# Optimization experiments

Measured on AMD Instinct MI355X. Metric: run time of the kernel, lower is better.

## Reference

```python
import jax, jax.numpy as jnp
import numpy as np

B, S, T = 512, 1024, 48
START, STOP, PAD = 45, 46, 47
NEG = -10000.0


def setup_inputs() -> dict:
    key = jax.random.key(0)
    k1, k2, k3, k4 = jax.random.split(key, 4)
    feats = jax.random.normal(k1, (B, S, T), dtype=jnp.float32)
    # contiguous-prefix masks (lengths in [1, S]) as the torch code assumes
    lengths = jax.random.randint(k2, (B,), 1, S + 1)
    masks = (jnp.arange(S)[None, :] < lengths[:, None]).astype(jnp.float32)
    tags = jax.random.randint(k3, (B, S), 0, T - 3)  # real tags only
    # transitions[i, j] = score of transitioning from tag j to tag i
    trans = jax.random.normal(k4, (T, T), dtype=jnp.float32)
    trans = trans.at[START, :].set(NEG)
    trans = trans.at[:, STOP].set(NEG)
    trans = trans.at[:, PAD].set(NEG)
    trans = trans.at[PAD, :].set(NEG)
    trans = trans.at[PAD, STOP].set(0.0)
    trans = trans.at[PAD, PAD].set(0.0)
    return {"feats": feats, "masks": masks, "tags": tags, "transitions": trans}


def _forward_algo(feats, masks, transitions):
    # feats [B,S,T], masks [B,S] -> partition log Z per sequence [B]
    score0 = jnp.full(feats.shape[::2], NEG, dtype=feats.dtype).at[:, START].set(0.0)

    def step(score, xs):
        emit, m = xs  # emit [B,T], m [B,1]
        # new[b,i] = LSE_j(score[b,j] + trans[i,j]) + emit[b,i]
        new = jax.nn.logsumexp(score[:, None, :] + transitions[None, :, :], axis=2) + emit
        return new * m + score * (1.0 - m), None

    xs = (jnp.swapaxes(feats, 0, 1), masks.T[:, :, None])
    score, _ = jax.lax.scan(step, score0, xs)
    return jax.nn.logsumexp(score + transitions[STOP][None, :], axis=1)


def _score_sentence(feats, masks, tags, transitions):
    # gold path score, vectorized over batch and time
    Bb = masks.shape[0]
    tags_ext = jnp.concatenate(
        [jnp.full((Bb, 1), START, dtype=tags.dtype), tags], axis=1)  # [B,S+1]
    emission = jnp.take_along_axis(feats, tags[:, :, None], axis=2)[:, :, 0]  # [B,S]
    trans_sc = transitions[tags_ext[:, 1:], tags_ext[:, :-1]]  # [B,S]
    score = jnp.sum((emission + trans_sc) * masks, axis=1)
    last_idx = masks.sum(1).astype(jnp.int32)  # length -> index into tags_ext
    last_tags = jnp.take_along_axis(tags_ext, last_idx[:, None], axis=1)[:, 0]
    return score + transitions[STOP, last_tags]


def reference(feats, masks, tags, transitions):
    # standard CRF negative log-likelihood per sequence: logZ - gold score
    return _forward_algo(feats, masks, transitions) - _score_sentence(
        feats, masks, tags, transitions)
```

## Files before the change

kernel.cpp:

```cpp
#include <hip/hip_runtime.h>
#include <cstdint>

constexpr int Sd = 1024;
constexpr int Td = 48;
constexpr int NTAG = 45;
constexpr int START_ = 45;
constexpr int STOP_ = 46;

typedef float v2f __attribute__((ext_vector_type(2)));

__device__ __forceinline__ int rfl_i(int x) { return __builtin_amdgcn_readfirstlane(x); }

#define ROTF(x, c) __int_as_float(__builtin_amdgcn_mov_dpp(__float_as_int(x), 0x120|(c), 0xF, 0xF, false))

#define STEP1(PF) do {                                                         \
    int _vi = __float_as_int(v);                                               \
    int _b1 = __builtin_amdgcn_ds_bpermute(a16, _vi);                          \
    int _b2 = __builtin_amdgcn_ds_bpermute(a32, _vi);                          \
    float _e = __expf(PF);                                                     \
    float g0v[16], g1v[16], g2v[16];                                           \
    g0v[0] = v;                                                                \
    g0v[1] = ROTF(g0v[0], 1);                                                  \
    g0v[2] = ROTF(g0v[0], 2);                                                  \
    g0v[3] = ROTF(g0v[1], 2);                                                  \
    _Pragma("unroll")                                                          \
    for (int i_ = 0; i_ < 4; ++i_) g0v[4+i_] = ROTF(g0v[i_], 4);               \
    _Pragma("unroll")                                                          \
    for (int i_ = 0; i_ < 8; ++i_) g0v[8+i_] = ROTF(g0v[i_], 8);               \
    g1v[0] = __int_as_float(_b1);                                              \
    g1v[1] = ROTF(g1v[0], 1);                                                  \
    g1v[2] = ROTF(g1v[0], 2);                                                  \
    g1v[3] = ROTF(g1v[1], 2);                                                  \
    _Pragma("unroll")                                                          \
    for (int i_ = 0; i_ < 4; ++i_) g1v[4+i_] = ROTF(g1v[i_], 4);               \
    _Pragma("unroll")                                                          \
    for (int i_ = 0; i_ < 8; ++i_) g1v[8+i_] = ROTF(g1v[i_], 8);               \
    g2v[0] = __int_as_float(_b2);                                              \
    g2v[1] = ROTF(g2v[0], 1);                                                  \
    g2v[2] = ROTF(g2v[0], 2);                                                  \
    g2v[3] = ROTF(g2v[1], 2);                                                  \
    _Pragma("unroll")                                                          \
    for (int i_ = 0; i_ < 4; ++i_) g2v[4+i_] = ROTF(g2v[i_], 4);               \
    _Pragma("unroll")                                                          \
    for (int i_ = 0; i_ < 8; ++i_) g2v[8+i_] = ROTF(g2v[i_], 8);               \
    v2f _ac0={0.f,0.f}, _ac1={0.f,0.f}, _ac2={0.f,0.f};                        \
    _Pragma("unroll")                                                          \
    for (int j_ = 0; j_ < 8; ++j_) {                                           \
        v2f _g0 = { g0v[2*j_], g0v[2*j_+1] };                                  \
        v2f _g1 = { g1v[2*j_], g1v[2*j_+1] };                                  \
        v2f _g2 = { g2v[2*j_], g2v[2*j_+1] };                                  \
        _ac0 = __builtin_elementwise_fma(epk[0][j_], _g0, _ac0);               \
        _ac1 = __builtin_elementwise_fma(epk[1][j_], _g1, _ac1);               \
        _ac2 = __builtin_elementwise_fma(epk[2][j_], _g2, _ac2);               \
    }                                                                          \
    v2f _s = _ac0 + (_ac1 + _ac2);                                             \
    float tot_ = _s.x + _s.y;                                                  \
    L += kx;                                                                   \
    uf = tot_ * sc;                                                            \
    v  = tot_ * (_e * sc);                                                     \
    { int _kb = rfl_i(__float_as_int(v));                                      \
      kx = ((_kb >> 23) & 0xFF) - 127;                                         \
      sc = __int_as_float((127 - kx) << 23); }                                 \
} while (0)

#define ADVP() do {                                                            \
    bool ok_ = isb ? (tn > 0) : (tn < tmax);                                   \
    pcur += ok_ ? sAdv : 0;                                                    \
    tn   += ok_ ? sInc : 0;                                                    \
} while (0)

__launch_bounds__(64, 1)
__global__ void crf_chains(const float* __restrict__ feats,
                           const float* __restrict__ masks,
                           const int* __restrict__ tags,
                           const float* __restrict__ trans,
                           float* __restrict__ wsv,
                           float* __restrict__ wsu,
                           int* __restrict__ wsLF, int* __restrict__ wsLB,
                           float* __restrict__ wsg,
                           int Bn)
{
    __shared__ float tl[Td * Td];
    const int lane = threadIdx.x;
    const bool isb = ((int)blockIdx.x >= Bn);
    const int b = isb ? ((int)blockIdx.x - Bn) : (int)blockIdx.x;

    for (int i = lane; i < Td * Td; i += 64) tl[i] = trans[i];
    __syncthreads();

    const size_t bS = (size_t)b * Sd;

    float c = 0.f;
    for (int t = lane; t < Sd; t += 64) c += masks[bS + t];
#pragma unroll
    for (int off = 32; off; off >>= 1) c += __shfl_xor(c, off);
    int len = (int)(c + 0.5f);
    if (len < 1) len = 1;
    len = rfl_i(len);

    if (!isb) {
        float g = 0.f;
        for (int t = lane; t < len; t += 64) {
            const int tag  = tags[bS + t];
            const int prev = (t == 0) ? START_ : tags[bS + t - 1];
            g += feats[(bS + t) * Td + tag] + tl[tag * Td + prev];
        }
#pragma unroll
        for (int off = 32; off; off >>= 1) g += __shfl_xor(g, off);
        g += tl[STOP_ * Td + tags[bS + len - 1]];
        if (lane == 0) wsg[b] = g;
    }

    const int p = lane & 15;
    const int qd = __builtin_amdgcn_mov_dpp(p, 0x121, 0xF, 0xF, false);
    const int d = (qd == ((p + 1) & 15)) ? 1 : -1;
    const int r0 = (lane >> 4) & 3;

    const int a16 = (((lane + 16) % Td) << 2);
    const int a32 = (((lane + 32) % Td) << 2);

    v2f epk[3][8];
#pragma unroll
    for (int h = 0; h < 3; ++h) {
        const int blk = 16 * ((r0 + h) % 3);
#pragma unroll
        for (int j = 0; j < 8; ++j) {
            const int c0 = blk + ((p + d * (2 * j))     & 15);
            const int c1 = blk + ((p + d * (2 * j + 1)) & 15);
            float e0 = 0.f, e1 = 0.f;
            if (!isb) {
                if (lane < NTAG) {
                    e0 = __expf(tl[lane * Td + c0]);
                    e1 = __expf(tl[lane * Td + c1]);
                }
            } else {
                if (lane < Td) {
                    e0 = __expf(tl[c0 * Td + lane]);
                    e1 = __expf(tl[c1 * Td + lane]);
                }
            }
            v2f ee = { e0, e1 };
            epk[h][j] = ee;
        }
    }

    const int lidx = (lane < Td) ? lane : 0;
    const float* frow = feats + bS * Td;
    const int Fh = (len + 1) >> 1;
    const int act = rfl_i(isb ? (len - Fh) : (Fh - 1));
    const int it0 = isb ? (len - 1) : 0;

    float einit;
    if (!isb) einit = (lane < NTAG) ? __expf(tl[lane * Td + START_]) : 0.f;
    else      einit = (lane < Td)   ? __expf(tl[STOP_ * Td + lane])  : 0.f;

    float v  = __expf(frow[(size_t)it0 * Td + lidx]) * einit;
    float uf = einit;
    int L = 0, kx; float sc;
    { int kb = rfl_i(__float_as_int(v)); kx = ((kb >> 23) & 0xFF) - 127;
      sc = __int_as_float((127 - kx) << 23); }

    auto eidx0 = [&](int s) -> int {
        if (!isb) { int t = 1 + s; return t < Sd ? t : (Sd - 1); }
        int t = len - 2 - s; return t > 0 ? t : 0;
    };
    float pf0 = frow[(size_t)eidx0(0) * Td + lidx];
    float pf1 = frow[(size_t)eidx0(1) * Td + lidx];
    float pf2 = frow[(size_t)eidx0(2) * Td + lidx];
    float pf3 = frow[(size_t)eidx0(3) * Td + lidx];
    float pf4 = frow[(size_t)eidx0(4) * Td + lidx];
    float pf5 = frow[(size_t)eidx0(5) * Td + lidx];
    float pf6 = frow[(size_t)eidx0(6) * Td + lidx];
    float pf7 = frow[(size_t)eidx0(7) * Td + lidx];
    int tn = eidx0(8);
    const float* pcur = frow + (size_t)tn * Td;
    const int sAdv = isb ? -Td : Td;
    const int sInc = isb ? -1 : 1;
    const int tmax = Sd - 1;

    int s = 0;
    while (s + 8 <= act) {
        STEP1(pf0); pf0 = pcur[lidx]; ADVP();
        STEP1(pf1); pf1 = pcur[lidx]; ADVP();
        STEP1(pf2); pf2 = pcur[lidx]; ADVP();
        STEP1(pf3); pf3 = pcur[lidx]; ADVP();
        STEP1(pf4); pf4 = pcur[lidx]; ADVP();
        STEP1(pf5); pf5 = pcur[lidx]; ADVP();
        STEP1(pf6); pf6 = pcur[lidx]; ADVP();
        STEP1(pf7); pf7 = pcur[lidx]; ADVP();
        s += 8;
    }
    if (s < act) { STEP1(pf0); ++s; }
    if (s < act) { STEP1(pf1); ++s; }
    if (s < act) { STEP1(pf2); ++s; }
    if (s < act) { STEP1(pf3); ++s; }
    if (s < act) { STEP1(pf4); ++s; }
    if (s < act) { STEP1(pf5); ++s; }
    if (s < act) { STEP1(pf6); ++s; }

    if (!isb) {
        if (lane < Td) wsv[lane * Bn + b] = v;
        if (lane == 0) wsLF[b] = L;
    } else {
        if (lane < Td) wsu[lane * Bn + b] = uf;
        if (lane == 0) wsLB[b] = L;
    }
}

__launch_bounds__(64)
__global__ void crf_combine(const float* __restrict__ wsv,
                            const float* __restrict__ wsu,
                            const int* __restrict__ wsLF,
                            const int* __restrict__ wsLB,
                            const float* __restrict__ wsg,
                            float* __restrict__ out, int Bn)
{
    const int b = blockIdx.x * 64 + threadIdx.x;
    if (b >= Bn) return;
    float dot = 0.f;
#pragma unroll
    for (int j = 0; j < Td; ++j)
        dot += wsv[j * Bn + b] * wsu[j * Bn + b];
    const float ln2 = 0.6931471805599453f;
    out[b] = (float)(wsLF[b] + wsLB[b]) * ln2 + __logf(dot) - wsg[b];
}

extern "C" void kernel_launch(void* const* d_in, const int* in_sizes, int n_in,
                              void* d_out, int out_size, void* d_ws, size_t ws_size,
                              hipStream_t stream) {
    const float* feats = (const float*)d_in[0];
    const float* masks = (const float*)d_in[1];
    const int*   tags  = (const int*)d_in[2];
    const float* trans = (const float*)d_in[3];
    float* outp = (float*)d_out;

    const int Bn = in_sizes[1] / Sd;

    float* wsv  = (float*)d_ws;
    float* wsu  = wsv + (size_t)Td * Bn;
    int*   wsLF = (int*)(wsu + (size_t)Td * Bn);
    int*   wsLB = wsLF + Bn;
    float* wsg  = (float*)(wsLB + Bn);

    crf_chains<<<dim3(2 * Bn), dim3(64), 0, stream>>>(feats, masks, tags, trans,
                                                      wsv, wsu, wsLF, wsLB, wsg, Bn);
    crf_combine<<<dim3((Bn + 63) / 64), dim3(64), 0, stream>>>(wsv, wsu, wsLF, wsLB, wsg, outp, Bn);
}
```

Before: 131.5 us.

## Fold DPP row rotations into FMA operands and hoist emission exp off the chain

Replaces the explicit DPP rotation tree and packed-FMA accumulation with inline-asm v_fmac_f32 instructions that apply row_ror directly to the source operand. Each slot is now 16 DPP-modified FMAs split across two accumulators, so the separate mov_dpp instructions are gone. The exp of the emission scores is computed when the prefetch is issued rather than inside the dependent step. This shortens the serial recurrence latency per time step, at the cost of losing packed v_pk_fma throughput and relying on inline asm that the compiler cannot schedule around.

```diff
diff --git a/kernel.cpp b/kernel.cpp
--- a/kernel.cpp
+++ b/kernel.cpp
@@ -7,57 +7,39 @@
 constexpr int START_ = 45;
 constexpr int STOP_ = 46;
 
-typedef float v2f __attribute__((ext_vector_type(2)));
-
 __device__ __forceinline__ int rfl_i(int x) { return __builtin_amdgcn_readfirstlane(x); }
 
-#define ROTF(x, c) __int_as_float(__builtin_amdgcn_mov_dpp(__float_as_int(x), 0x120|(c), 0xF, 0xF, false))
+#define FMD(acc, s, ee, N) \
+    asm("v_fmac_f32 %0, %1, %2 row_ror:" #N " row_mask:0xf bank_mask:0xf" \
+        : "+v"(acc) : "v"(s), "v"(ee))
+#define MULD(acc, s, ee, N) \
+    asm("v_mul_f32 %0, %1, %2 row_ror:" #N " row_mask:0xf bank_mask:0xf" \
+        : "=v"(acc) : "v"(s), "v"(ee))
+
+#define SLOT16(s, E, aA, aB) do {                                              \
+    aA = (s) * E[0];                                                           \
+    FMD(aA, s, E[1], 1);  FMD(aA, s, E[2], 2);  FMD(aA, s, E[3], 3);           \
+    FMD(aA, s, E[4], 4);  FMD(aA, s, E[5], 5);  FMD(aA, s, E[6], 6);           \
+    FMD(aA, s, E[7], 7);                                                       \
+    MULD(aB, s, E[8], 8);                                                      \
+    FMD(aB, s, E[9], 9);  FMD(aB, s, E[10], 10); FMD(aB, s, E[11], 11);        \
+    FMD(aB, s, E[12], 12); FMD(aB, s, E[13], 13); FMD(aB, s, E[14], 14);       \
+    FMD(aB, s, E[15], 15);                                                     \
+} while (0)
 
 #define STEP1(PF) do {                                                         \
     int _vi = __float_as_int(v);                                               \
     int _b1 = __builtin_amdgcn_ds_bpermute(a16, _vi);                          \
     int _b2 = __builtin_amdgcn_ds_bpermute(a32, _vi);                          \
-    float _e = __expf(PF);                                                     \
-    float g0v[16], g1v[16], g2v[16];                                           \
-    g0v[0] = v;                                                                \
-    g0v[1] = ROTF(g0v[0], 1);                                                  \
-    g0v[2] = ROTF(g0v[0], 2);                                                  \
-    g0v[3] = ROTF(g0v[1], 2);                                                  \
-    _Pragma("unroll")                                                          \
-    for (int i_ = 0; i_ < 4; ++i_) g0v[4+i_] = ROTF(g0v[i_], 4);               \
-    _Pragma("unroll")                                                          \
-    for (int i_ = 0; i_ < 8; ++i_) g0v[8+i_] = ROTF(g0v[i_], 8);               \
-    g1v[0] = __int_as_float(_b1);                                              \
-    g1v[1] = ROTF(g1v[0], 1);                                                  \
-    g1v[2] = ROTF(g1v[0], 2);                                                  \
-    g1v[3] = ROTF(g1v[1], 2);                                                  \
-    _Pragma("unroll")                                                          \
-    for (int i_ = 0; i_ < 4; ++i_) g1v[4+i_] = ROTF(g1v[i_], 4);               \
-    _Pragma("unroll")                                                          \
-    for (int i_ = 0; i_ < 8; ++i_) g1v[8+i_] = ROTF(g1v[i_], 8);               \
-    g2v[0] = __int_as_float(_b2);                                              \
-    g2v[1] = ROTF(g2v[0], 1);                                                  \
-    g2v[2] = ROTF(g2v[0], 2);                                                  \
-    g2v[3] = ROTF(g2v[1], 2);                                                  \
-    _Pragma("unroll")                                                          \
-    for (int i_ = 0; i_ < 4; ++i_) g2v[4+i_] = ROTF(g2v[i_], 4);               \
-    _Pragma("unroll")                                                          \
-    for (int i_ = 0; i_ < 8; ++i_) g2v[8+i_] = ROTF(g2v[i_], 8);               \
-    v2f _ac0={0.f,0.f}, _ac1={0.f,0.f}, _ac2={0.f,0.f};                        \
-    _Pragma("unroll")                                                          \
-    for (int j_ = 0; j_ < 8; ++j_) {                                           \
-        v2f _g0 = { g0v[2*j_], g0v[2*j_+1] };                                  \
-        v2f _g1 = { g1v[2*j_], g1v[2*j_+1] };                                  \
-        v2f _g2 = { g2v[2*j_], g2v[2*j_+1] };                                  \
-        _ac0 = __builtin_elementwise_fma(epk[0][j_], _g0, _ac0);               \
-        _ac1 = __builtin_elementwise_fma(epk[1][j_], _g1, _ac1);               \
-        _ac2 = __builtin_elementwise_fma(epk[2][j_], _g2, _ac2);               \
-    }                                                                          \
-    v2f _s = _ac0 + (_ac1 + _ac2);                                             \
-    float tot_ = _s.x + _s.y;                                                  \
+    float _s1 = __int_as_float(_b1), _s2 = __int_as_float(_b2);                \
+    float a0A, a0B, a1A, a1B, a2A, a2B;                                        \
+    SLOT16(v,   eA0, a0A, a0B);                                                \
+    SLOT16(_s1, eA1, a1A, a1B);                                                \
+    SLOT16(_s2, eA2, a2A, a2B);                                                \
+    float tot_ = ((a0A + a0B) + (a1A + a1B)) + (a2A + a2B);                    \
     L += kx;                                                                   \
     uf = tot_ * sc;                                                            \
-    v  = tot_ * (_e * sc);                                                     \
+    v  = tot_ * ((PF) * sc);                                                   \
     { int _kb = rfl_i(__float_as_int(v));                                      \
       kx = ((_kb >> 23) & 0xFF) - 127;                                         \
       sc = __int_as_float((127 - kx) << 23); }                                 \
@@ -119,28 +101,21 @@
     const int a16 = (((lane + 16) % Td) << 2);
     const int a32 = (((lane + 32) % Td) << 2);
 
-    v2f epk[3][8];
+    float eA0[16], eA1[16], eA2[16];
 #pragma unroll
     for (int h = 0; h < 3; ++h) {
+        float* dst = (h == 0) ? eA0 : (h == 1) ? eA1 : eA2;
         const int blk = 16 * ((r0 + h) % 3);
 #pragma unroll
-        for (int j = 0; j < 8; ++j) {
-            const int c0 = blk + ((p + d * (2 * j))     & 15);
-            const int c1 = blk + ((p + d * (2 * j + 1)) & 15);
-            float e0 = 0.f, e1 = 0.f;
+        for (int i = 0; i < 16; ++i) {
+            const int cc = blk + ((p + d * i) & 15);
+            float e0 = 0.f;
             if (!isb) {
-                if (lane < NTAG) {
-                    e0 = __expf(tl[lane * Td + c0]);
-                    e1 = __expf(tl[lane * Td + c1]);
-                }
+                if (lane < NTAG) e0 = __expf(tl[lane * Td + cc]);
             } else {
-                if (lane < Td) {
-                    e0 = __expf(tl[c0 * Td + lane]);
-                    e1 = __expf(tl[c1 * Td + lane]);
-                }
+                if (lane < Td)   e0 = __expf(tl[cc * Td + lane]);
             }
-            v2f ee = { e0, e1 };
-            epk[h][j] = ee;
+            dst[i] = e0;
         }
     }
 
@@ -164,14 +139,14 @@
         if (!isb) { int t = 1 + s; return t < Sd ? t : (Sd - 1); }
         int t = len - 2 - s; return t > 0 ? t : 0;
     };
-    float pf0 = frow[(size_t)eidx0(0) * Td + lidx];
-    float pf1 = frow[(size_t)eidx0(1) * Td + lidx];
-    float pf2 = frow[(size_t)eidx0(2) * Td + lidx];
-    float pf3 = frow[(size_t)eidx0(3) * Td + lidx];
-    float pf4 = frow[(size_t)eidx0(4) * Td + lidx];
-    float pf5 = frow[(size_t)eidx0(5) * Td + lidx];
-    float pf6 = frow[(size_t)eidx0(6) * Td + lidx];
-    float pf7 = frow[(size_t)eidx0(7) * Td + lidx];
+    float pf0 = __expf(frow[(size_t)eidx0(0) * Td + lidx]);
+    float pf1 = __expf(frow[(size_t)eidx0(1) * Td + lidx]);
+    float pf2 = __expf(frow[(size_t)eidx0(2) * Td + lidx]);
+    float pf3 = __expf(frow[(size_t)eidx0(3) * Td + lidx]);
+    float pf4 = __expf(frow[(size_t)eidx0(4) * Td + lidx]);
+    float pf5 = __expf(frow[(size_t)eidx0(5) * Td + lidx]);
+    float pf6 = __expf(frow[(size_t)eidx0(6) * Td + lidx]);
+    float pf7 = __expf(frow[(size_t)eidx0(7) * Td + lidx]);
     int tn = eidx0(8);
     const float* pcur = frow + (size_t)tn * Td;
     const int sAdv = isb ? -Td : Td;
@@ -180,14 +155,14 @@
 
     int s = 0;
     while (s + 8 <= act) {
-        STEP1(pf0); pf0 = pcur[lidx]; ADVP();
-        STEP1(pf1); pf1 = pcur[lidx]; ADVP();
-        STEP1(pf2); pf2 = pcur[lidx]; ADVP();
-        STEP1(pf3); pf3 = pcur[lidx]; ADVP();
-        STEP1(pf4); pf4 = pcur[lidx]; ADVP();
-        STEP1(pf5); pf5 = pcur[lidx]; ADVP();
-        STEP1(pf6); pf6 = pcur[lidx]; ADVP();
-        STEP1(pf7); pf7 = pcur[lidx]; ADVP();
+        STEP1(pf0); pf0 = __expf(pcur[lidx]); ADVP();
+        STEP1(pf1); pf1 = __expf(pcur[lidx]); ADVP();
+        STEP1(pf2); pf2 = __expf(pcur[lidx]); ADVP();
+        STEP1(pf3); pf3 = __expf(pcur[lidx]); ADVP();
+        STEP1(pf4); pf4 = __expf(pcur[lidx]); ADVP();
+        STEP1(pf5); pf5 = __expf(pcur[lidx]); ADVP();
+        STEP1(pf6); pf6 = __expf(pcur[lidx]); ADVP();
+        STEP1(pf7); pf7 = __expf(pcur[lidx]); ADVP();
         s += 8;
     }
     if (s < act) { STEP1(pf0); ++s; }
```

Result: faster. 119.1 us (-9.5%).
